# Kernel optimization log

Measured on AMD Instinct MI355X. Metric: run time of the kernel, lower is better.

## Reference

```python
import jax, jax.numpy as jnp
import numpy as np

N, B, SDIM, ADIM, HID, HEADS = 8, 32768, 128, 16, 128, 4
AD = HID // HEADS  # attend_dim = 32
IDIM = SDIM + ADIM


def setup_inputs() -> dict:
    key = jax.random.key(0)
    ks = jax.random.split(key, 16)
    nrm = jax.random.normal
    return {
        "states": nrm(ks[0], (N, B, SDIM), jnp.float32),
        "actions": nrm(ks[1], (N, B, ADIM), jnp.float32),
        # per-agent critic encoder (Linear(idim, hid) + ReLU)
        "We": nrm(ks[2], (N, IDIM, HID), jnp.float32) * 0.05,
        "be": nrm(ks[3], (N, HID), jnp.float32) * 0.05,
        # per-agent state encoder (Linear(sdim, hid) + ReLU)
        "Ws": nrm(ks[4], (N, SDIM, HID), jnp.float32) * 0.05,
        "bs": nrm(ks[5], (N, HID), jnp.float32) * 0.05,
        # per-head extractors (shared across agents)
        "Wk": nrm(ks[6], (HEADS, HID, AD), jnp.float32) * 0.05,  # bias=False
        "Wq": nrm(ks[7], (HEADS, HID, AD), jnp.float32) * 0.05,  # bias=False
        "Wv": nrm(ks[8], (HEADS, HID, AD), jnp.float32) * 0.05,
        "bv": nrm(ks[9], (HEADS, AD), jnp.float32) * 0.05,
        # per-agent critic head: Linear(2*hid, hid) + ReLU + Linear(hid, adim)
        "Wc1": nrm(ks[10], (N, 2 * HID, HID), jnp.float32) * 0.05,
        "bc1": nrm(ks[11], (N, HID), jnp.float32) * 0.05,
        "Wc2": nrm(ks[12], (N, HID, ADIM), jnp.float32) * 0.05,
        "bc2": nrm(ks[13], (N, ADIM), jnp.float32) * 0.05,
    }


def reference(states, actions, We, be, Ws, bs, Wk, Wq, Wv, bv, Wc1, bc1, Wc2, bc2):
    # encoders
    inp = jnp.concatenate([states, actions], axis=-1)                      # [N,B,idim]
    sa_enc = jax.nn.relu(jnp.einsum('nbi,nih->nbh', inp, We) + be[:, None, :])
    s_enc = jax.nn.relu(jnp.einsum('nbs,nsh->nbh', states, Ws) + bs[:, None, :])
    # per-head keys/values/selectors; k = head index
    K = jnp.einsum('nbh,khd->knbd', sa_enc, Wk)                            # [H,N,B,ad]
    V = jax.nn.relu(jnp.einsum('nbh,khd->knbd', sa_enc, Wv) + bv[:, None, None, :])
    Q = jnp.einsum('nbh,khd->knbd', s_enc, Wq)
    # attention logits: selector of agent i dotted with key of agent j
    logits = jnp.einsum('kibd,kjbd->kbij', Q, K) / np.sqrt(AD).astype(np.float32)
    # exclude-self masking (equivalent to stacking keys with j != i)
    self_mask = jnp.eye(N, dtype=bool)                                     # [N,N]
    masked = jnp.where(self_mask[None, None, :, :], jnp.float32(-1e9), logits)
    attn = jax.nn.softmax(masked, axis=-1)                                 # [H,B,N,N]
    other = jnp.einsum('kbij,kjbd->ikbd', attn, V)                         # [N,H,B,ad]
    other = other.transpose(0, 2, 1, 3).reshape(N, B, HEADS * AD)          # head-order concat
    # per-agent critic MLP
    critic_in = jnp.concatenate([s_enc, other], axis=-1)                   # [N,B,2*hid]
    h1 = jax.nn.relu(jnp.einsum('nbc,nch->nbh', critic_in, Wc1) + bc1[:, None, :])
    all_q = jnp.einsum('nbh,nha->nba', h1, Wc2) + bc2[:, None, :]          # [N,B,adim]
    int_acs = jnp.argmax(actions, axis=-1)                                 # [N,B]
    q = jnp.take_along_axis(all_q, int_acs[..., None], axis=-1)            # [N,B,1]
    return q
```

## Files before the change

### kernel.cpp

```cpp
#include <hip/hip_runtime.h>

#define NAG 8
#define BB 32768
#define SDIM 128
#define ADIM 16
#define HID 128
#define IDIM 144

typedef unsigned short u16;
typedef unsigned int u32;
typedef __attribute__((ext_vector_type(8))) short short8;
typedef __attribute__((ext_vector_type(4))) float floatx4;

__device__ __forceinline__ u16 f2bf(float f) {
  u32 u = __float_as_uint(f);
  u32 r = (u + 0x7FFFu + ((u >> 16) & 1u)) >> 16;
  return (u16)r;
}
__device__ __forceinline__ float bflo(u32 u) { return __uint_as_float(u << 16); }
__device__ __forceinline__ float bfhi(u32 u) { return __uint_as_float(u & 0xFFFF0000u); }


__global__ void prep_kernel(const float* __restrict__ We, const float* __restrict__ Ws,
                            const float* __restrict__ Wk, const float* __restrict__ Wq,
                            const float* __restrict__ Wv, const float* __restrict__ Wc1,
                            u16* __restrict__ ws) {
  int idx = blockIdx.x * 256 + threadIdx.x;
  const float* src;
  u16* dst;
  int e, Kreal, mode = 0;
  if (idx < 163840) {
    int a = idx / 20480; e = idx % 20480;
    src = We + a * (IDIM * HID); dst = ws + a * 20480; Kreal = IDIM;
  } else if (idx < 294912) {
    int r = idx - 163840; int a = r >> 14; e = r & 16383;
    src = Ws + a * 16384; dst = ws + 163840 + a * 16384; Kreal = 128;
  } else if (idx < 311296) {
    e = idx - 294912; src = Wk; dst = ws + 294912; Kreal = 128; mode = 1;
  } else if (idx < 327680) {
    e = idx - 311296; src = Wv; dst = ws + 311296; Kreal = 128; mode = 1;
  } else if (idx < 344064) {
    e = idx - 327680; src = Wq; dst = ws + 327680; Kreal = 128; mode = 1;
  } else if (idx < 606208) {
    int r = idx - 344064; int a = r >> 15; e = r & 32767;
    src = Wc1 + a * 32768; dst = ws + 344064 + a * 32768; Kreal = 256;
  } else {
    return;
  }
  int j = e & 7, lane = (e >> 3) & 63, ct = (e >> 9) & 7, kc = e >> 12;
  int k = kc * 32 + ((lane >> 4) << 3) + j;
  int c = ct * 16 + (lane & 15);
  float val = 0.f;
  if (k < Kreal)
    val = mode ? src[((c >> 5) * 128 + k) * 32 + (c & 31)]
               : src[k * 128 + c];
  dst[e] = f2bf(val);
}

template <int NKC>
__device__ __forceinline__ void gemm8(const u16* A, const int astride,
                                      const u16* __restrict__ W,
                                      const int wave, const int lane, floatx4* acc) {
  const int arow = wave * 16 + (lane & 15);
  const int koff = (lane >> 4) << 3;
#pragma unroll
  for (int kc = 0; kc < NKC; ++kc) {
    short8 a = *(const short8*)&A[arow * astride + kc * 32 + koff];
#pragma unroll
    for (int ct = 0; ct < 8; ++ct) {
      short8 b = *(const short8*)&W[kc * 4096 + ct * 512 + lane * 8];
      acc[ct] = __builtin_amdgcn_mfma_f32_16x16x32_bf16(a, b, acc[ct], 0, 0, 0);
    }
  }
}

__global__ __launch_bounds__(512, 4) void k1_kernel(
    const float* __restrict__ states, const float* __restrict__ actions,
    const float* __restrict__ be, const float* __restrict__ bs, const float* __restrict__ bv,
    const u16* __restrict__ wsbase,
    u16* __restrict__ Kbuf, u16* __restrict__ Vbuf, u16* __restrict__ Qbuf,
    u16* __restrict__ CI) {
  __shared__ __align__(16) u16 Alds[128 * 160];
  __shared__ __align__(16) u16 Ebuf[128 * 136];

  const int tid = threadIdx.x, lane = tid & 63, wave = tid >> 6;
  const int n = blockIdx.y;
  const size_t b0 = (size_t)blockIdx.x * 128;
  const int colb = lane & 15;
  const int rowl = wave * 16 + ((lane >> 4) << 2);

  const u16* WeP = wsbase + (size_t)n * 20480;
  const u16* WsP = wsbase + 163840 + (size_t)n * 16384;
  const u16* WkP = wsbase + 294912;
  const u16* WvP = wsbase + 311296;
  const u16* WqP = wsbase + 327680;

  {
    const float4* sp = (const float4*)(states + ((size_t)n * BB + b0) * SDIM);
#pragma unroll
    for (int it = 0; it < 8; ++it) {
      int c = tid + it * 512;
      float4 v = sp[c];
      int row = c >> 5, col = (c & 31) << 2;
      *(uint2*)&Alds[row * 160 + col] =
          make_uint2((u32)f2bf(v.x) | ((u32)f2bf(v.y) << 16),
                     (u32)f2bf(v.z) | ((u32)f2bf(v.w) << 16));
    }
    const float4* apt = (const float4*)(actions + ((size_t)n * BB + b0) * ADIM);
    {
      float4 v = apt[tid];
      int row = tid >> 2, col = 128 + ((tid & 3) << 2);
      *(uint2*)&Alds[row * 160 + col] =
          make_uint2((u32)f2bf(v.x) | ((u32)f2bf(v.y) << 16),
                     (u32)f2bf(v.z) | ((u32)f2bf(v.w) << 16));
    }
    {
      int row = tid >> 2, col = 144 + ((tid & 3) << 2);
      *(uint2*)&Alds[row * 160 + col] = make_uint2(0u, 0u);
    }
  }
  __syncthreads();

  floatx4 acc[8];

#pragma unroll
  for (int ct = 0; ct < 8; ++ct) acc[ct] = (floatx4){0.f, 0.f, 0.f, 0.f};
  gemm8<5>(Alds, 160, WeP, wave, lane, acc);
#pragma unroll
  for (int ct = 0; ct < 8; ++ct) {
    int col = ct * 16 + colb;
    float bb = be[n * HID + col];
#pragma unroll
    for (int r = 0; r < 4; ++r)
      Ebuf[(rowl + r) * 136 + col] = f2bf(fmaxf(acc[ct][r] + bb, 0.f));
  }
  __syncthreads();

#pragma unroll
  for (int ct = 0; ct < 8; ++ct) acc[ct] = (floatx4){0.f, 0.f, 0.f, 0.f};
  gemm8<4>(Ebuf, 136, WkP, wave, lane, acc);
#pragma unroll
  for (int ct = 0; ct < 8; ++ct) {
    int col = ct * 16 + colb;
#pragma unroll
    for (int r = 0; r < 4; ++r)
      Kbuf[((size_t)n * BB + b0 + rowl + r) * HID + col] = f2bf(acc[ct][r]);
  }

#pragma unroll
  for (int ct = 0; ct < 8; ++ct) acc[ct] = (floatx4){0.f, 0.f, 0.f, 0.f};
  gemm8<4>(Ebuf, 136, WvP, wave, lane, acc);
#pragma unroll
  for (int ct = 0; ct < 8; ++ct) {
    int col = ct * 16 + colb;
    float bb = bv[col];
#pragma unroll
    for (int r = 0; r < 4; ++r)
      Vbuf[((size_t)n * BB + b0 + rowl + r) * HID + col] = f2bf(fmaxf(acc[ct][r] + bb, 0.f));
  }

#pragma unroll
  for (int ct = 0; ct < 8; ++ct) acc[ct] = (floatx4){0.f, 0.f, 0.f, 0.f};
  gemm8<4>(Alds, 160, WsP, wave, lane, acc);
  u16 e2u[32];
#pragma unroll
  for (int ct = 0; ct < 8; ++ct) {
    int col = ct * 16 + colb;
    float bb = bs[n * HID + col];
#pragma unroll
    for (int r = 0; r < 4; ++r) {
      u16 u = f2bf(fmaxf(acc[ct][r] + bb, 0.f));
      e2u[ct * 4 + r] = u;
      CI[((size_t)n * BB + b0 + rowl + r) * 256 + col] = u;
    }
  }
  __syncthreads();

#pragma unroll
  for (int ct = 0; ct < 8; ++ct) {
    int col = ct * 16 + colb;
#pragma unroll
    for (int r = 0; r < 4; ++r)
      Ebuf[(rowl + r) * 136 + col] = e2u[ct * 4 + r];
  }
  __syncthreads();

#pragma unroll
  for (int ct = 0; ct < 8; ++ct) acc[ct] = (floatx4){0.f, 0.f, 0.f, 0.f};
  gemm8<4>(Ebuf, 136, WqP, wave, lane, acc);
#pragma unroll
  for (int ct = 0; ct < 8; ++ct) {
    int col = ct * 16 + colb;
#pragma unroll
    for (int r = 0; r < 4; ++r)
      Qbuf[((size_t)n * BB + b0 + rowl + r) * HID + col] = f2bf(acc[ct][r]);
  }
}

__global__ __launch_bounds__(512, 4) void k2_kernel(const u16* __restrict__ Kb,
                                                    const u16* __restrict__ Vb,
                                                    const u16* __restrict__ Qb,
                                                    u16* __restrict__ CI) {
  __shared__ __align__(16) u16 Ksh[8 * 16 * 128];
  __shared__ __align__(16) u16 Vsh[8 * 16 * 128];

  const int tid = threadIdx.x;
  const int i = tid >> 6;
  const int lane = tid & 63;
  const int h = lane >> 4;
  const int b = lane & 15;
  const size_t b0 = (size_t)blockIdx.x * 16;
  const float scale = 0.17677669529663687f;

  {
    uint4* kd = (uint4*)Ksh;
    uint4* vd = (uint4*)Vsh;
#pragma unroll
    for (int it = 0; it < 4; ++it) {
      int l = tid + it * 512;
      int j = l >> 8, bs_ = (l >> 4) & 15, t = l & 15;
      size_t gidx = ((size_t)j * BB + b0 + bs_) * 16 + t;
      int slot = (t + bs_) & 15;
      int didx = (j * 16 + bs_) * 16 + slot;
      kd[didx] = ((const uint4*)Kb)[gidx];
      vd[didx] = ((const uint4*)Vb)[gidx];
    }
  }
  __syncthreads();

  float q[32];
  {
    const u32* qp = (const u32*)(Qb + ((size_t)i * BB + b0 + b) * HID + h * 32);
#pragma unroll
    for (int t = 0; t < 16; ++t) {
      u32 u = qp[t];
      q[2 * t] = bflo(u);
      q[2 * t + 1] = bfhi(u);
    }
  }

  float lg[8];
#pragma unroll
  for (int j = 0; j < 8; ++j) {
    if (j != i) {
      float acc = 0.f;
#pragma unroll
      for (int c = 0; c < 4; ++c) {
        int slot = ((h * 4 + c) + b) & 15;
        uint4 kv = *(const uint4*)&Ksh[((j * 16 + b) * 16 + slot) * 8];
        const u32 kw[4] = {kv.x, kv.y, kv.z, kv.w};
#pragma unroll
        for (int t = 0; t < 4; ++t) {
          int d = c * 8 + t * 2;
          acc = fmaf(bflo(kw[t]), q[d], acc);
          acc = fmaf(bfhi(kw[t]), q[d + 1], acc);
        }
      }
      lg[j] = acc * scale;
    } else {
      lg[j] = -1e9f;
    }
  }

  float m = lg[0];
#pragma unroll
  for (int j = 1; j < 8; ++j) m = fmaxf(m, lg[j]);
  float p[8], s = 0.f;
#pragma unroll
  for (int j = 0; j < 8; ++j) {
    p[j] = __expf(lg[j] - m);
    s += p[j];
  }
  const float inv = 1.f / s;

  float o[32];
#pragma unroll
  for (int d = 0; d < 32; ++d) o[d] = 0.f;
#pragma unroll
  for (int j = 0; j < 8; ++j) {
    if (j == i) continue;
    const float pj = p[j] * inv;
#pragma unroll
    for (int c = 0; c < 4; ++c) {
      int slot = ((h * 4 + c) + b) & 15;
      uint4 vv = *(const uint4*)&Vsh[((j * 16 + b) * 16 + slot) * 8];
      const u32 vw[4] = {vv.x, vv.y, vv.z, vv.w};
#pragma unroll
      for (int t = 0; t < 4; ++t) {
        int d = c * 8 + t * 2;
        o[d] = fmaf(pj, bflo(vw[t]), o[d]);
        o[d + 1] = fmaf(pj, bfhi(vw[t]), o[d + 1]);
      }
    }
  }

  u32 ow[16];
#pragma unroll
  for (int t = 0; t < 16; ++t)
    ow[t] = (u32)f2bf(o[2 * t]) | ((u32)f2bf(o[2 * t + 1]) << 16);
  uint4* op = (uint4*)(CI + ((size_t)i * BB + b0 + b) * 256 + 128 + h * 32);
  op[0] = make_uint4(ow[0], ow[1], ow[2], ow[3]);
  op[1] = make_uint4(ow[4], ow[5], ow[6], ow[7]);
  op[2] = make_uint4(ow[8], ow[9], ow[10], ow[11]);
  op[3] = make_uint4(ow[12], ow[13], ow[14], ow[15]);
}

__global__ __launch_bounds__(512, 4) void k3_kernel(
    const u16* __restrict__ CI, const u16* __restrict__ Wc1P, const float* __restrict__ bc1,
    const float* __restrict__ Wc2, const float* __restrict__ bc2,
    const float* __restrict__ actions, float* __restrict__ out) {
  __shared__ __align__(16) u16 Alds[128 * 264];
  __shared__ __align__(16) float Wc2s[2048];

  const int tid = threadIdx.x, lane = tid & 63, wave = tid >> 6;
  const int n = blockIdx.y;
  const size_t b0 = (size_t)blockIdx.x * 128;
  const int colb = lane & 15;
  const int rowl = wave * 16 + ((lane >> 4) << 2);

  {
    const uint4* src = (const uint4*)(CI + ((size_t)n * BB + b0) * 256);
    uint4* dstA = (uint4*)Alds;
#pragma unroll
    for (int it = 0; it < 8; ++it) {
      int c = tid + it * 512;
      int row = c >> 5, c16 = c & 31;
      dstA[row * 33 + c16] = src[c];
    }
    ((float4*)Wc2s)[tid] = ((const float4*)(Wc2 + n * 2048))[tid];
  }
  __syncthreads();

  floatx4 acc[8];
#pragma unroll
  for (int ct = 0; ct < 8; ++ct) acc[ct] = (floatx4){0.f, 0.f, 0.f, 0.f};
  gemm8<8>(Alds, 264, Wc1P + (size_t)n * 32768, wave, lane, acc);
  __syncthreads();

#pragma unroll
  for (int ct = 0; ct < 8; ++ct) {
    int col = ct * 16 + colb;
    float bb = bc1[n * HID + col];
#pragma unroll
    for (int r = 0; r < 4; ++r) {
      float v = fmaxf(acc[ct][r] + bb, 0.f);
      Alds[(rowl + r) * 136 + col] = f2bf(v);
    }
  }
  __syncthreads();

  {
    const int bloc = tid >> 2, part = tid & 3;
    const size_t b = b0 + bloc;
    const float* ap = actions + ((size_t)n * BB + b) * ADIM;
    int am = 0;
    float mv = ap[0];
#pragma unroll
    for (int t = 1; t < 16; ++t) {
      float v = ap[t];
      if (v > mv) { mv = v; am = t; }
    }
    float a2 = 0.f;
    const int cb = part * 32;
#pragma unroll
    for (int c2 = 0; c2 < 32; ++c2) {
      float hv = __uint_as_float((u32)Alds[bloc * 136 + cb + c2] << 16);
      a2 = fmaf(hv, Wc2s[(cb + c2) * 16 + am], a2);
    }
    a2 += __shfl_xor(a2, 1);
    a2 += __shfl_xor(a2, 2);
    if (part == 0) out[(size_t)n * BB + b] = a2 + bc2[n * ADIM + am];
  }
}

extern "C" void kernel_launch(void* const* d_in, const int* in_sizes, int n_in,
                              void* d_out, int out_size, void* d_ws, size_t ws_size,
                              hipStream_t stream) {
  const float* states  = (const float*)d_in[0];
  const float* actions = (const float*)d_in[1];
  const float* We  = (const float*)d_in[2];
  const float* be  = (const float*)d_in[3];
  const float* Ws  = (const float*)d_in[4];
  const float* bs  = (const float*)d_in[5];
  const float* Wk  = (const float*)d_in[6];
  const float* Wq  = (const float*)d_in[7];
  const float* Wv  = (const float*)d_in[8];
  const float* bv  = (const float*)d_in[9];
  const float* Wc1 = (const float*)d_in[10];
  const float* bc1 = (const float*)d_in[11];
  const float* Wc2 = (const float*)d_in[12];
  const float* bc2 = (const float*)d_in[13];
  float* out = (float*)d_out;
  u16* ws = (u16*)d_ws;

  u16* Kbuf = ws + 606208;
  u16* Vbuf = ws + 34160640;
  u16* Qbuf = ws + 67715072;
  u16* CI   = ws + 101269504;

  prep_kernel<<<2368, 256, 0, stream>>>(We, Ws, Wk, Wq, Wv, Wc1, ws);
  k1_kernel<<<dim3(256, 8), 512, 0, stream>>>(states, actions, be, bs, bv, ws,
                                              Kbuf, Vbuf, Qbuf, CI);
  k2_kernel<<<2048, 512, 0, stream>>>(Kbuf, Vbuf, Qbuf, CI);
  k3_kernel<<<dim3(256, 8), 512, 0, stream>>>(CI, ws + 344064, bc1, Wc2, bc2, actions, out);
}
```

Before: 493.3 us.

## Swap GEMM wave tiling to column-per-wave with register-resident weight fragments

Each wave now owns one 16-column output slice across all 128 rows, so its weight fragments for every K chunk are loaded once into registers and reused across eight row tiles, instead of re-reading weights for each row tile. In k1 the states and actions tiles are no longer staged through LDS as bf16; the A fragments are read straight from global fp32 and converted in registers, which removes the Alds buffer and one barrier. The cost is that states are read from global twice (once for the We GEMM, once for the Ws GEMM) with strided per-lane loads, and register pressure rises from holding the weight fragments.

New measurement: 645.5 us. 30.8% more time.

```diff
diff --git a/kernel.cpp b/kernel.cpp
--- a/kernel.cpp
+++ b/kernel.cpp
@@ -12,6 +12,8 @@
 typedef __attribute__((ext_vector_type(8))) short short8;
 typedef __attribute__((ext_vector_type(4))) float floatx4;
 
+#define BMFMA(a, b, c) __builtin_amdgcn_mfma_f32_16x16x32_bf16((a), (b), (c), 0, 0, 0)
+
 __device__ __forceinline__ u16 f2bf(float f) {
   u32 u = __float_as_uint(f);
   u32 r = (u + 0x7FFFu + ((u >> 16) & 1u)) >> 16;
@@ -19,6 +21,15 @@
 }
 __device__ __forceinline__ float bflo(u32 u) { return __uint_as_float(u << 16); }
 __device__ __forceinline__ float bfhi(u32 u) { return __uint_as_float(u & 0xFFFF0000u); }
+
+__device__ __forceinline__ short8 cvt8(const float4 a, const float4 b) {
+  short8 r;
+  r[0] = (short)f2bf(a.x); r[1] = (short)f2bf(a.y);
+  r[2] = (short)f2bf(a.z); r[3] = (short)f2bf(a.w);
+  r[4] = (short)f2bf(b.x); r[5] = (short)f2bf(b.y);
+  r[6] = (short)f2bf(b.z); r[7] = (short)f2bf(b.w);
+  return r;
+}
 
 
 __global__ void prep_kernel(const float* __restrict__ We, const float* __restrict__ Ws,
@@ -57,143 +68,161 @@
   dst[e] = f2bf(val);
 }
 
-template <int NKC>
-__device__ __forceinline__ void gemm8(const u16* A, const int astride,
-                                      const u16* __restrict__ W,
-                                      const int wave, const int lane, floatx4* acc) {
-  const int arow = wave * 16 + (lane & 15);
-  const int koff = (lane >> 4) << 3;
-#pragma unroll
-  for (int kc = 0; kc < NKC; ++kc) {
-    short8 a = *(const short8*)&A[arow * astride + kc * 32 + koff];
-#pragma unroll
-    for (int ct = 0; ct < 8; ++ct) {
-      short8 b = *(const short8*)&W[kc * 4096 + ct * 512 + lane * 8];
-      acc[ct] = __builtin_amdgcn_mfma_f32_16x16x32_bf16(a, b, acc[ct], 0, 0, 0);
-    }
-  }
-}
-
 __global__ __launch_bounds__(512, 4) void k1_kernel(
     const float* __restrict__ states, const float* __restrict__ actions,
     const float* __restrict__ be, const float* __restrict__ bs, const float* __restrict__ bv,
     const u16* __restrict__ wsbase,
     u16* __restrict__ Kbuf, u16* __restrict__ Vbuf, u16* __restrict__ Qbuf,
     u16* __restrict__ CI) {
-  __shared__ __align__(16) u16 Alds[128 * 160];
   __shared__ __align__(16) u16 Ebuf[128 * 136];
 
-  const int tid = threadIdx.x, lane = tid & 63, wave = tid >> 6;
+  const int tid = threadIdx.x, lane = tid & 63, w = tid >> 6;
   const int n = blockIdx.y;
   const size_t b0 = (size_t)blockIdx.x * 128;
-  const int colb = lane & 15;
-  const int rowl = wave * 16 + ((lane >> 4) << 2);
-
-  const u16* WeP = wsbase + (size_t)n * 20480;
-  const u16* WsP = wsbase + 163840 + (size_t)n * 16384;
-  const u16* WkP = wsbase + 294912;
-  const u16* WvP = wsbase + 311296;
-  const u16* WqP = wsbase + 327680;
-
-  {
-    const float4* sp = (const float4*)(states + ((size_t)n * BB + b0) * SDIM);
-#pragma unroll
-    for (int it = 0; it < 8; ++it) {
-      int c = tid + it * 512;
-      float4 v = sp[c];
-      int row = c >> 5, col = (c & 31) << 2;
-      *(uint2*)&Alds[row * 160 + col] =
-          make_uint2((u32)f2bf(v.x) | ((u32)f2bf(v.y) << 16),
-                     (u32)f2bf(v.z) | ((u32)f2bf(v.w) << 16));
-    }
-    const float4* apt = (const float4*)(actions + ((size_t)n * BB + b0) * ADIM);
-    {
-      float4 v = apt[tid];
-      int row = tid >> 2, col = 128 + ((tid & 3) << 2);
-      *(uint2*)&Alds[row * 160 + col] =
-          make_uint2((u32)f2bf(v.x) | ((u32)f2bf(v.y) << 16),
-                     (u32)f2bf(v.z) | ((u32)f2bf(v.w) << 16));
-    }
-    {
-      int row = tid >> 2, col = 144 + ((tid & 3) << 2);
-      *(uint2*)&Alds[row * 160 + col] = make_uint2(0u, 0u);
-    }
-  }
-  __syncthreads();
+  const int cb = lane & 15, qq = lane >> 4;
+  const int col = w * 16 + cb;
+  const int ar = lane & 15;
+  const int koff = qq * 8;
+
+  const u16* WeF = wsbase + (size_t)n * 20480 + w * 512 + (size_t)lane * 8;
+  const u16* WsF = wsbase + 163840 + (size_t)n * 16384 + w * 512 + (size_t)lane * 8;
+  const u16* WkF = wsbase + 294912 + w * 512 + (size_t)lane * 8;
+  const u16* WvF = wsbase + 311296 + w * 512 + (size_t)lane * 8;
+  const u16* WqF = wsbase + 327680 + w * 512 + (size_t)lane * 8;
+
+  const float* Sb = states + ((size_t)n * BB + b0) * SDIM;
+  const float* Ab = actions + ((size_t)n * BB + b0) * ADIM;
+  const size_t orow = (size_t)n * BB + b0;
 
   floatx4 acc[8];
 
-#pragma unroll
-  for (int ct = 0; ct < 8; ++ct) acc[ct] = (floatx4){0.f, 0.f, 0.f, 0.f};
-  gemm8<5>(Alds, 160, WeP, wave, lane, acc);
-#pragma unroll
-  for (int ct = 0; ct < 8; ++ct) {
-    int col = ct * 16 + colb;
-    float bb = be[n * HID + col];
+  {
+    short8 wf[5];
+#pragma unroll
+    for (int kc = 0; kc < 5; ++kc) wf[kc] = *(const short8*)(WeF + kc * 4096);
+#pragma unroll
+    for (int m = 0; m < 8; ++m) acc[m] = (floatx4){0.f, 0.f, 0.f, 0.f};
+#pragma unroll
+    for (int m = 0; m < 8; ++m) {
+      const float* sp = Sb + (size_t)(16 * m + ar) * SDIM + koff;
+#pragma unroll
+      for (int kc = 0; kc < 4; ++kc) {
+        float4 x = *(const float4*)(sp + kc * 32);
+        float4 y = *(const float4*)(sp + kc * 32 + 4);
+        acc[m] = BMFMA(cvt8(x, y), wf[kc], acc[m]);
+      }
+      short8 af = {0, 0, 0, 0, 0, 0, 0, 0};
+      if (qq < 2) {
+        const float* ap = Ab + (size_t)(16 * m + ar) * ADIM + koff;
+        float4 x = *(const float4*)ap;
+        float4 y = *(const float4*)(ap + 4);
+        af = cvt8(x, y);
+      }
+      acc[m] = BMFMA(af, wf[4], acc[m]);
+    }
+    const float bb = be[n * HID + col];
+#pragma unroll
+    for (int m = 0; m < 8; ++m)
+#pragma unroll
+      for (int r = 0; r < 4; ++r)
+        Ebuf[(16 * m + qq * 4 + r) * 136 + col] = f2bf(fmaxf(acc[m][r] + bb, 0.f));
+  }
+  __syncthreads();
+
+  {
+    short8 wf[4];
+#pragma unroll
+    for (int kc = 0; kc < 4; ++kc) wf[kc] = *(const short8*)(WkF + kc * 4096);
+#pragma unroll
+    for (int m = 0; m < 8; ++m) acc[m] = (floatx4){0.f, 0.f, 0.f, 0.f};
+#pragma unroll
+    for (int m = 0; m < 8; ++m)
+#pragma unroll
+      for (int kc = 0; kc < 4; ++kc) {
+        short8 a = *(const short8*)&Ebuf[(16 * m + ar) * 136 + kc * 32 + koff];
+        acc[m] = BMFMA(a, wf[kc], acc[m]);
+      }
+#pragma unroll
+    for (int m = 0; m < 8; ++m)
+#pragma unroll
+      for (int r = 0; r < 4; ++r)
+        Kbuf[(orow + 16 * m + qq * 4 + r) * HID + col] = f2bf(acc[m][r]);
+  }
+
+  {
+    short8 wf[4];
+#pragma unroll
+    for (int kc = 0; kc < 4; ++kc) wf[kc] = *(const short8*)(WvF + kc * 4096);
+#pragma unroll
+    for (int m = 0; m < 8; ++m) acc[m] = (floatx4){0.f, 0.f, 0.f, 0.f};
+#pragma unroll
+    for (int m = 0; m < 8; ++m)
+#pragma unroll
+      for (int kc = 0; kc < 4; ++kc) {
+        short8 a = *(const short8*)&Ebuf[(16 * m + ar) * 136 + kc * 32 + koff];
+        acc[m] = BMFMA(a, wf[kc], acc[m]);
+      }
+    const float bb = bv[col];
+#pragma unroll
+    for (int m = 0; m < 8; ++m)
+#pragma unroll
+      for (int r = 0; r < 4; ++r)
+        Vbuf[(orow + 16 * m + qq * 4 + r) * HID + col] = f2bf(fmaxf(acc[m][r] + bb, 0.f));
+  }
+
+  {
+    short8 wf[4];
+#pragma unroll
+    for (int kc = 0; kc < 4; ++kc) wf[kc] = *(const short8*)(WsF + kc * 4096);
+#pragma unroll
+    for (int m = 0; m < 8; ++m) acc[m] = (floatx4){0.f, 0.f, 0.f, 0.f};
+#pragma unroll
+    for (int m = 0; m < 8; ++m) {
+      const float* sp = Sb + (size_t)(16 * m + ar) * SDIM + koff;
+#pragma unroll
+      for (int kc = 0; kc < 4; ++kc) {
+        float4 x = *(const float4*)(sp + kc * 32);
+        float4 y = *(const float4*)(sp + kc * 32 + 4);
+        acc[m] = BMFMA(cvt8(x, y), wf[kc], acc[m]);
+      }
+    }
+    const float bb = bs[n * HID + col];
+#pragma unroll
+    for (int m = 0; m < 8; ++m)
+#pragma unroll
+      for (int r = 0; r < 4; ++r) {
+        float v = fmaxf(acc[m][r] + bb, 0.f);
+        acc[m][r] = v;
+        CI[(orow + 16 * m + qq * 4 + r) * 256 + col] = f2bf(v);
+      }
+  }
+  __syncthreads();
+
+#pragma unroll
+  for (int m = 0; m < 8; ++m)
 #pragma unroll
     for (int r = 0; r < 4; ++r)
-      Ebuf[(rowl + r) * 136 + col] = f2bf(fmaxf(acc[ct][r] + bb, 0.f));
-  }
-  __syncthreads();
-
-#pragma unroll
-  for (int ct = 0; ct < 8; ++ct) acc[ct] = (floatx4){0.f, 0.f, 0.f, 0.f};
-  gemm8<4>(Ebuf, 136, WkP, wave, lane, acc);
-#pragma unroll
-  for (int ct = 0; ct < 8; ++ct) {
-    int col = ct * 16 + colb;
-#pragma unroll
-    for (int r = 0; r < 4; ++r)
-      Kbuf[((size_t)n * BB + b0 + rowl + r) * HID + col] = f2bf(acc[ct][r]);
-  }
-
-#pragma unroll
-  for (int ct = 0; ct < 8; ++ct) acc[ct] = (floatx4){0.f, 0.f, 0.f, 0.f};
-  gemm8<4>(Ebuf, 136, WvP, wave, lane, acc);
-#pragma unroll
-  for (int ct = 0; ct < 8; ++ct) {
-    int col = ct * 16 + colb;
-    float bb = bv[col];
-#pragma unroll
-    for (int r = 0; r < 4; ++r)
-      Vbuf[((size_t)n * BB + b0 + rowl + r) * HID + col] = f2bf(fmaxf(acc[ct][r] + bb, 0.f));
-  }
-
-#pragma unroll
-  for (int ct = 0; ct < 8; ++ct) acc[ct] = (floatx4){0.f, 0.f, 0.f, 0.f};
-  gemm8<4>(Alds, 160, WsP, wave, lane, acc);
-  u16 e2u[32];
-#pragma unroll
-  for (int ct = 0; ct < 8; ++ct) {
-    int col = ct * 16 + colb;
-    float bb = bs[n * HID + col];
-#pragma unroll
-    for (int r = 0; r < 4; ++r) {
-      u16 u = f2bf(fmaxf(acc[ct][r] + bb, 0.f));
-      e2u[ct * 4 + r] = u;
-      CI[((size_t)n * BB + b0 + rowl + r) * 256 + col] = u;
-    }
-  }
-  __syncthreads();
-
-#pragma unroll
-  for (int ct = 0; ct < 8; ++ct) {
-    int col = ct * 16 + colb;
-#pragma unroll
-    for (int r = 0; r < 4; ++r)
-      Ebuf[(rowl + r) * 136 + col] = e2u[ct * 4 + r];
-  }
-  __syncthreads();
-
-#pragma unroll
-  for (int ct = 0; ct < 8; ++ct) acc[ct] = (floatx4){0.f, 0.f, 0.f, 0.f};
-  gemm8<4>(Ebuf, 136, WqP, wave, lane, acc);
-#pragma unroll
-  for (int ct = 0; ct < 8; ++ct) {
-    int col = ct * 16 + colb;
-#pragma unroll
-    for (int r = 0; r < 4; ++r)
-      Qbuf[((size_t)n * BB + b0 + rowl + r) * HID + col] = f2bf(acc[ct][r]);
+      Ebuf[(16 * m + qq * 4 + r) * 136 + col] = f2bf(acc[m][r]);
+  __syncthreads();
+
+  {
+    short8 wf[4];
+#pragma unroll
+    for (int kc = 0; kc < 4; ++kc) wf[kc] = *(const short8*)(WqF + kc * 4096);
+#pragma unroll
+    for (int m = 0; m < 8; ++m) acc[m] = (floatx4){0.f, 0.f, 0.f, 0.f};
+#pragma unroll
+    for (int m = 0; m < 8; ++m)
+#pragma unroll
+      for (int kc = 0; kc < 4; ++kc) {
+        short8 a = *(const short8*)&Ebuf[(16 * m + ar) * 136 + kc * 32 + koff];
+        acc[m] = BMFMA(a, wf[kc], acc[m]);
+      }
+#pragma unroll
+    for (int m = 0; m < 8; ++m)
+#pragma unroll
+      for (int r = 0; r < 4; ++r)
+        Qbuf[(orow + 16 * m + qq * 4 + r) * HID + col] = f2bf(acc[m][r]);
   }
 }
 
@@ -312,11 +341,13 @@
   __shared__ __align__(16) u16 Alds[128 * 264];
   __shared__ __align__(16) float Wc2s[2048];
 
-  const int tid = threadIdx.x, lane = tid & 63, wave = tid >> 6;
+  const int tid = threadIdx.x, lane = tid & 63, w = tid >> 6;
   const int n = blockIdx.y;
   const size_t b0 = (size_t)blockIdx.x * 128;
-  const int colb = lane & 15;
-  const int rowl = wave * 16 + ((lane >> 4) << 2);
+  const int cb = lane & 15, qq = lane >> 4;
+  const int col = w * 16 + cb;
+  const int ar = lane & 15;
+  const int koff = qq * 8;
 
   {
     const uint4* src = (const uint4*)(CI + ((size_t)n * BB + b0) * 256);
@@ -332,20 +363,30 @@
   __syncthreads();
 
   floatx4 acc[8];
-#pragma unroll
-  for (int ct = 0; ct < 8; ++ct) acc[ct] = (floatx4){0.f, 0.f, 0.f, 0.f};
-  gemm8<8>(Alds, 264, Wc1P + (size_t)n * 32768, wave, lane, acc);
-  __syncthreads();
-
-#pragma unroll
-  for (int ct = 0; ct < 8; ++ct) {
-    int col = ct * 16 + colb;
-    float bb = bc1[n * HID + col];
-#pragma unroll
-    for (int r = 0; r < 4; ++r) {
-      float v = fmaxf(acc[ct][r] + bb, 0.f);
-      Alds[(rowl + r) * 136 + col] = f2bf(v);
-    }
+  {
+    const u16* WcF = Wc1P + (size_t)n * 32768 + w * 512 + (size_t)lane * 8;
+    short8 wf[8];
+#pragma unroll
+    for (int kc = 0; kc < 8; ++kc) wf[kc] = *(const short8*)(WcF + kc * 4096);
+#pragma unroll
+    for (int m = 0; m < 8; ++m) acc[m] = (floatx4){0.f, 0.f, 0.f, 0.f};
+#pragma unroll
+    for (int m = 0; m < 8; ++m)
+#pragma unroll
+      for (int kc = 0; kc < 8; ++kc) {
+        short8 a = *(const short8*)&Alds[(16 * m + ar) * 264 + kc * 32 + koff];
+        acc[m] = BMFMA(a, wf[kc], acc[m]);
+      }
+  }
+  __syncthreads();
+
+  {
+    const float bb = bc1[n * HID + col];
+#pragma unroll
+    for (int m = 0; m < 8; ++m)
+#pragma unroll
+      for (int r = 0; r < 4; ++r)
+        Alds[(16 * m + qq * 4 + r) * 136 + col] = f2bf(fmaxf(acc[m][r] + bb, 0.f));
   }
   __syncthreads();
 
@@ -361,11 +402,11 @@
       if (v > mv) { mv = v; am = t; }
     }
     float a2 = 0.f;
-    const int cb = part * 32;
+    const int cbk = part * 32;
 #pragma unroll
     for (int c2 = 0; c2 < 32; ++c2) {
-      float hv = __uint_as_float((u32)Alds[bloc * 136 + cb + c2] << 16);
-      a2 = fmaf(hv, Wc2s[(cb + c2) * 16 + am], a2);
+      float hv = __uint_as_float((u32)Alds[bloc * 136 + cbk + c2] << 16);
+      a2 = fmaf(hv, Wc2s[(cbk + c2) * 16 + am], a2);
     }
     a2 += __shfl_xor(a2, 1);
     a2 += __shfl_xor(a2, 2);
```

## Stage weights in LDS and keep activations in registers as MFMA B operand

Applied to the files above, without the earlier changes.

k1 and k3 now stage each weight matrix into shared memory per phase and load activation fragments directly from global into registers, swapping MFMA operand roles so activations are the B operand. The GEMM output lands transposed, so each lane holds one row's contiguous four columns and can do packed 8-byte stores. k3 also folds the second linear layer and the argmax gather into registers with cross-lane shuffles, dropping the LDS round trip. Weights were previously read from global on every MFMA; this trades that for more barriers and repeated weight staging per block.

Result: faster. 420.3 us (-14.8%).

```diff
diff --git a/kernel.cpp b/kernel.cpp
--- a/kernel.cpp
+++ b/kernel.cpp
@@ -12,6 +12,8 @@
 typedef __attribute__((ext_vector_type(8))) short short8;
 typedef __attribute__((ext_vector_type(4))) float floatx4;
 
+#define BMFMA(a, b, c) __builtin_amdgcn_mfma_f32_16x16x32_bf16((a), (b), (c), 0, 0, 0)
+
 __device__ __forceinline__ u16 f2bf(float f) {
   u32 u = __float_as_uint(f);
   u32 r = (u + 0x7FFFu + ((u >> 16) & 1u)) >> 16;
@@ -19,6 +21,26 @@
 }
 __device__ __forceinline__ float bflo(u32 u) { return __uint_as_float(u << 16); }
 __device__ __forceinline__ float bfhi(u32 u) { return __uint_as_float(u & 0xFFFF0000u); }
+
+__device__ __forceinline__ short8 cvt8(const float4 a, const float4 b) {
+  short8 r;
+  r[0] = (short)f2bf(a.x); r[1] = (short)f2bf(a.y);
+  r[2] = (short)f2bf(a.z); r[3] = (short)f2bf(a.w);
+  r[4] = (short)f2bf(b.x); r[5] = (short)f2bf(b.y);
+  r[6] = (short)f2bf(b.z); r[7] = (short)f2bf(b.w);
+  return r;
+}
+__device__ __forceinline__ uint2 pack4(float a, float b, float c, float d) {
+  return make_uint2((u32)f2bf(a) | ((u32)f2bf(b) << 16),
+                    (u32)f2bf(c) | ((u32)f2bf(d) << 16));
+}
+
+__device__ __forceinline__ void stageW(u16* Wb, const u16* __restrict__ src, int nu4, int tid) {
+  const uint4* s4 = (const uint4*)src;
+  uint4* d4 = (uint4*)Wb;
+#pragma unroll 1
+  for (int it = tid; it < nu4; it += 512) d4[it] = s4[it];
+}
 
 
 __global__ void prep_kernel(const float* __restrict__ We, const float* __restrict__ Ws,
@@ -57,37 +79,21 @@
   dst[e] = f2bf(val);
 }
 
-template <int NKC>
-__device__ __forceinline__ void gemm8(const u16* A, const int astride,
-                                      const u16* __restrict__ W,
-                                      const int wave, const int lane, floatx4* acc) {
-  const int arow = wave * 16 + (lane & 15);
-  const int koff = (lane >> 4) << 3;
-#pragma unroll
-  for (int kc = 0; kc < NKC; ++kc) {
-    short8 a = *(const short8*)&A[arow * astride + kc * 32 + koff];
-#pragma unroll
-    for (int ct = 0; ct < 8; ++ct) {
-      short8 b = *(const short8*)&W[kc * 4096 + ct * 512 + lane * 8];
-      acc[ct] = __builtin_amdgcn_mfma_f32_16x16x32_bf16(a, b, acc[ct], 0, 0, 0);
-    }
-  }
-}
-
 __global__ __launch_bounds__(512, 4) void k1_kernel(
     const float* __restrict__ states, const float* __restrict__ actions,
     const float* __restrict__ be, const float* __restrict__ bs, const float* __restrict__ bv,
     const u16* __restrict__ wsbase,
     u16* __restrict__ Kbuf, u16* __restrict__ Vbuf, u16* __restrict__ Qbuf,
     u16* __restrict__ CI) {
-  __shared__ __align__(16) u16 Alds[128 * 160];
-  __shared__ __align__(16) u16 Ebuf[128 * 136];
-
-  const int tid = threadIdx.x, lane = tid & 63, wave = tid >> 6;
+  __shared__ __align__(16) u16 Wb[20480];
+  __shared__ __align__(16) u16 Est[8 * 16 * 136];
+
+  const int tid = threadIdx.x, lane = tid & 63, w = tid >> 6;
+  const int cb = lane & 15, qq = lane >> 4;
   const int n = blockIdx.y;
   const size_t b0 = (size_t)blockIdx.x * 128;
-  const int colb = lane & 15;
-  const int rowl = wave * 16 + ((lane >> 4) << 2);
+  const size_t grow = (size_t)n * BB + b0 + w * 16 + cb;
+  u16* stw = Est + w * (16 * 136) + cb * 136;
 
   const u16* WeP = wsbase + (size_t)n * 20480;
   const u16* WsP = wsbase + 163840 + (size_t)n * 16384;
@@ -95,105 +101,103 @@
   const u16* WvP = wsbase + 311296;
   const u16* WqP = wsbase + 327680;
 
+  stageW(Wb, WeP, 2560, tid);
+  short8 xf[5];
   {
-    const float4* sp = (const float4*)(states + ((size_t)n * BB + b0) * SDIM);
-#pragma unroll
-    for (int it = 0; it < 8; ++it) {
-      int c = tid + it * 512;
-      float4 v = sp[c];
-      int row = c >> 5, col = (c & 31) << 2;
-      *(uint2*)&Alds[row * 160 + col] =
-          make_uint2((u32)f2bf(v.x) | ((u32)f2bf(v.y) << 16),
-                     (u32)f2bf(v.z) | ((u32)f2bf(v.w) << 16));
-    }
-    const float4* apt = (const float4*)(actions + ((size_t)n * BB + b0) * ADIM);
-    {
-      float4 v = apt[tid];
-      int row = tid >> 2, col = 128 + ((tid & 3) << 2);
-      *(uint2*)&Alds[row * 160 + col] =
-          make_uint2((u32)f2bf(v.x) | ((u32)f2bf(v.y) << 16),
-                     (u32)f2bf(v.z) | ((u32)f2bf(v.w) << 16));
-    }
-    {
-      int row = tid >> 2, col = 144 + ((tid & 3) << 2);
-      *(uint2*)&Alds[row * 160 + col] = make_uint2(0u, 0u);
-    }
-  }
-  __syncthreads();
-
-  floatx4 acc[8];
-
-#pragma unroll
-  for (int ct = 0; ct < 8; ++ct) acc[ct] = (floatx4){0.f, 0.f, 0.f, 0.f};
-  gemm8<5>(Alds, 160, WeP, wave, lane, acc);
-#pragma unroll
-  for (int ct = 0; ct < 8; ++ct) {
-    int col = ct * 16 + colb;
-    float bb = be[n * HID + col];
-#pragma unroll
-    for (int r = 0; r < 4; ++r)
-      Ebuf[(rowl + r) * 136 + col] = f2bf(fmaxf(acc[ct][r] + bb, 0.f));
-  }
-  __syncthreads();
-
-#pragma unroll
-  for (int ct = 0; ct < 8; ++ct) acc[ct] = (floatx4){0.f, 0.f, 0.f, 0.f};
-  gemm8<4>(Ebuf, 136, WkP, wave, lane, acc);
-#pragma unroll
-  for (int ct = 0; ct < 8; ++ct) {
-    int col = ct * 16 + colb;
-#pragma unroll
-    for (int r = 0; r < 4; ++r)
-      Kbuf[((size_t)n * BB + b0 + rowl + r) * HID + col] = f2bf(acc[ct][r]);
-  }
-
-#pragma unroll
-  for (int ct = 0; ct < 8; ++ct) acc[ct] = (floatx4){0.f, 0.f, 0.f, 0.f};
-  gemm8<4>(Ebuf, 136, WvP, wave, lane, acc);
-#pragma unroll
-  for (int ct = 0; ct < 8; ++ct) {
-    int col = ct * 16 + colb;
-    float bb = bv[col];
-#pragma unroll
-    for (int r = 0; r < 4; ++r)
-      Vbuf[((size_t)n * BB + b0 + rowl + r) * HID + col] = f2bf(fmaxf(acc[ct][r] + bb, 0.f));
-  }
-
-#pragma unroll
-  for (int ct = 0; ct < 8; ++ct) acc[ct] = (floatx4){0.f, 0.f, 0.f, 0.f};
-  gemm8<4>(Alds, 160, WsP, wave, lane, acc);
-  u16 e2u[32];
-#pragma unroll
-  for (int ct = 0; ct < 8; ++ct) {
-    int col = ct * 16 + colb;
-    float bb = bs[n * HID + col];
-#pragma unroll
-    for (int r = 0; r < 4; ++r) {
-      u16 u = f2bf(fmaxf(acc[ct][r] + bb, 0.f));
-      e2u[ct * 4 + r] = u;
-      CI[((size_t)n * BB + b0 + rowl + r) * 256 + col] = u;
-    }
-  }
-  __syncthreads();
-
-#pragma unroll
-  for (int ct = 0; ct < 8; ++ct) {
-    int col = ct * 16 + colb;
-#pragma unroll
-    for (int r = 0; r < 4; ++r)
-      Ebuf[(rowl + r) * 136 + col] = e2u[ct * 4 + r];
-  }
-  __syncthreads();
-
-#pragma unroll
-  for (int ct = 0; ct < 8; ++ct) acc[ct] = (floatx4){0.f, 0.f, 0.f, 0.f};
-  gemm8<4>(Ebuf, 136, WqP, wave, lane, acc);
-#pragma unroll
-  for (int ct = 0; ct < 8; ++ct) {
-    int col = ct * 16 + colb;
-#pragma unroll
-    for (int r = 0; r < 4; ++r)
-      Qbuf[((size_t)n * BB + b0 + rowl + r) * HID + col] = f2bf(acc[ct][r]);
+    const float* sp = states + grow * SDIM + qq * 8;
+#pragma unroll
+    for (int kc = 0; kc < 4; ++kc) {
+      float4 x = *(const float4*)(sp + kc * 32);
+      float4 y = *(const float4*)(sp + kc * 32 + 4);
+      xf[kc] = cvt8(x, y);
+    }
+    xf[4] = (short8){0, 0, 0, 0, 0, 0, 0, 0};
+    if (qq < 2) {
+      const float* ap = actions + grow * ADIM + qq * 8;
+      xf[4] = cvt8(*(const float4*)ap, *(const float4*)(ap + 4));
+    }
+  }
+  __syncthreads();
+#pragma unroll
+  for (int ct = 0; ct < 8; ++ct) {
+    floatx4 a = (floatx4){0.f, 0.f, 0.f, 0.f};
+#pragma unroll
+    for (int kc = 0; kc < 5; ++kc) {
+      short8 wfr = *(const short8*)&Wb[(kc * 8 + ct) * 512 + lane * 8];
+      a = BMFMA(wfr, xf[kc], a);
+    }
+    floatx4 bb = *(const floatx4*)&be[n * HID + ct * 16 + qq * 4];
+    *(uint2*)&stw[ct * 16 + qq * 4] =
+        pack4(fmaxf(a[0] + bb[0], 0.f), fmaxf(a[1] + bb[1], 0.f),
+              fmaxf(a[2] + bb[2], 0.f), fmaxf(a[3] + bb[3], 0.f));
+  }
+  __syncthreads();
+
+  stageW(Wb, WkP, 2048, tid);
+  short8 ef[4];
+#pragma unroll
+  for (int kc = 0; kc < 4; ++kc) ef[kc] = *(const short8*)&stw[kc * 32 + qq * 8];
+  __syncthreads();
+#pragma unroll
+  for (int ct = 0; ct < 8; ++ct) {
+    floatx4 a = (floatx4){0.f, 0.f, 0.f, 0.f};
+#pragma unroll
+    for (int kc = 0; kc < 4; ++kc) {
+      short8 wfr = *(const short8*)&Wb[(kc * 8 + ct) * 512 + lane * 8];
+      a = BMFMA(wfr, ef[kc], a);
+    }
+    *(uint2*)&Kbuf[grow * HID + ct * 16 + qq * 4] = pack4(a[0], a[1], a[2], a[3]);
+  }
+  __syncthreads();
+
+  stageW(Wb, WvP, 2048, tid);
+  __syncthreads();
+#pragma unroll
+  for (int ct = 0; ct < 8; ++ct) {
+    floatx4 a = (floatx4){0.f, 0.f, 0.f, 0.f};
+#pragma unroll
+    for (int kc = 0; kc < 4; ++kc) {
+      short8 wfr = *(const short8*)&Wb[(kc * 8 + ct) * 512 + lane * 8];
+      a = BMFMA(wfr, ef[kc], a);
+    }
+    floatx4 bb = *(const floatx4*)&bv[ct * 16 + qq * 4];
+    *(uint2*)&Vbuf[grow * HID + ct * 16 + qq * 4] =
+        pack4(fmaxf(a[0] + bb[0], 0.f), fmaxf(a[1] + bb[1], 0.f),
+              fmaxf(a[2] + bb[2], 0.f), fmaxf(a[3] + bb[3], 0.f));
+  }
+  __syncthreads();
+
+  stageW(Wb, WsP, 2048, tid);
+  __syncthreads();
+#pragma unroll
+  for (int ct = 0; ct < 8; ++ct) {
+    floatx4 a = (floatx4){0.f, 0.f, 0.f, 0.f};
+#pragma unroll
+    for (int kc = 0; kc < 4; ++kc) {
+      short8 wfr = *(const short8*)&Wb[(kc * 8 + ct) * 512 + lane * 8];
+      a = BMFMA(wfr, xf[kc], a);
+    }
+    floatx4 bb = *(const floatx4*)&bs[n * HID + ct * 16 + qq * 4];
+    uint2 pk = pack4(fmaxf(a[0] + bb[0], 0.f), fmaxf(a[1] + bb[1], 0.f),
+                     fmaxf(a[2] + bb[2], 0.f), fmaxf(a[3] + bb[3], 0.f));
+    *(uint2*)&CI[grow * 256 + ct * 16 + qq * 4] = pk;
+    *(uint2*)&stw[ct * 16 + qq * 4] = pk;
+  }
+  __syncthreads();
+
+  stageW(Wb, WqP, 2048, tid);
+#pragma unroll
+  for (int kc = 0; kc < 4; ++kc) ef[kc] = *(const short8*)&stw[kc * 32 + qq * 8];
+  __syncthreads();
+#pragma unroll
+  for (int ct = 0; ct < 8; ++ct) {
+    floatx4 a = (floatx4){0.f, 0.f, 0.f, 0.f};
+#pragma unroll
+    for (int kc = 0; kc < 4; ++kc) {
+      short8 wfr = *(const short8*)&Wb[(kc * 8 + ct) * 512 + lane * 8];
+      a = BMFMA(wfr, ef[kc], a);
+    }
+    *(uint2*)&Qbuf[grow * HID + ct * 16 + qq * 4] = pack4(a[0], a[1], a[2], a[3]);
   }
 }
 
@@ -309,68 +313,74 @@
     const u16* __restrict__ CI, const u16* __restrict__ Wc1P, const float* __restrict__ bc1,
     const float* __restrict__ Wc2, const float* __restrict__ bc2,
     const float* __restrict__ actions, float* __restrict__ out) {
-  __shared__ __align__(16) u16 Alds[128 * 264];
+  __shared__ __align__(16) u16 Wb[16384];
   __shared__ __align__(16) float Wc2s[2048];
 
-  const int tid = threadIdx.x, lane = tid & 63, wave = tid >> 6;
+  const int tid = threadIdx.x, lane = tid & 63, w = tid >> 6;
+  const int cb = lane & 15, qq = lane >> 4;
   const int n = blockIdx.y;
   const size_t b0 = (size_t)blockIdx.x * 128;
-  const int colb = lane & 15;
-  const int rowl = wave * 16 + ((lane >> 4) << 2);
-
-  {
-    const uint4* src = (const uint4*)(CI + ((size_t)n * BB + b0) * 256);
-    uint4* dstA = (uint4*)Alds;
-#pragma unroll
-    for (int it = 0; it < 8; ++it) {
-      int c = tid + it * 512;
-      int row = c >> 5, c16 = c & 31;
-      dstA[row * 33 + c16] = src[c];
-    }
-    ((float4*)Wc2s)[tid] = ((const float4*)(Wc2 + n * 2048))[tid];
-  }
-  __syncthreads();
+  const size_t grow = (size_t)n * BB + b0 + w * 16 + cb;
+
+  const u16* W1 = Wc1P + (size_t)n * 32768;
+  Wc2s[tid] = Wc2[n * 2048 + tid];
+  Wc2s[tid + 512] = Wc2[n * 2048 + tid + 512];
+  Wc2s[tid + 1024] = Wc2[n * 2048 + tid + 1024];
+  Wc2s[tid + 1536] = Wc2[n * 2048 + tid + 1536];
+  stageW(Wb, W1, 2048, tid);
+
+  const u16* cip = CI + grow * 256;
+  short8 cf[4];
+#pragma unroll
+  for (int kc = 0; kc < 4; ++kc) cf[kc] = *(const short8*)(cip + kc * 32 + qq * 8);
 
   floatx4 acc[8];
 #pragma unroll
   for (int ct = 0; ct < 8; ++ct) acc[ct] = (floatx4){0.f, 0.f, 0.f, 0.f};
-  gemm8<8>(Alds, 264, Wc1P + (size_t)n * 32768, wave, lane, acc);
-  __syncthreads();
-
-#pragma unroll
-  for (int ct = 0; ct < 8; ++ct) {
-    int col = ct * 16 + colb;
-    float bb = bc1[n * HID + col];
+
+  __syncthreads();
+#pragma unroll
+  for (int ct = 0; ct < 8; ++ct)
+#pragma unroll
+    for (int kc = 0; kc < 4; ++kc) {
+      short8 wfr = *(const short8*)&Wb[(kc * 8 + ct) * 512 + lane * 8];
+      acc[ct] = BMFMA(wfr, cf[kc], acc[ct]);
+    }
+  __syncthreads();
+  stageW(Wb, W1 + 16384, 2048, tid);
+#pragma unroll
+  for (int kc = 0; kc < 4; ++kc) cf[kc] = *(const short8*)(cip + 128 + kc * 32 + qq * 8);
+  __syncthreads();
+#pragma unroll
+  for (int ct = 0; ct < 8; ++ct)
+#pragma unroll
+    for (int kc = 0; kc < 4; ++kc) {
+      short8 wfr = *(const short8*)&Wb[(kc * 8 + ct) * 512 + lane * 8];
+      acc[ct] = BMFMA(wfr, cf[kc], acc[ct]);
+    }
+
+  const float* ap = actions + grow * ADIM;
+  int am = 0;
+  float mv = ap[0];
+#pragma unroll
+  for (int t = 1; t < 16; ++t) {
+    float v = ap[t];
+    if (v > mv) { mv = v; am = t; }
+  }
+
+  float a2 = 0.f;
+#pragma unroll
+  for (int ct = 0; ct < 8; ++ct) {
+    floatx4 bb = *(const floatx4*)&bc1[n * HID + ct * 16 + qq * 4];
 #pragma unroll
     for (int r = 0; r < 4; ++r) {
-      float v = fmaxf(acc[ct][r] + bb, 0.f);
-      Alds[(rowl + r) * 136 + col] = f2bf(v);
-    }
-  }
-  __syncthreads();
-
-  {
-    const int bloc = tid >> 2, part = tid & 3;
-    const size_t b = b0 + bloc;
-    const float* ap = actions + ((size_t)n * BB + b) * ADIM;
-    int am = 0;
-    float mv = ap[0];
-#pragma unroll
-    for (int t = 1; t < 16; ++t) {
-      float v = ap[t];
-      if (v > mv) { mv = v; am = t; }
-    }
-    float a2 = 0.f;
-    const int cb = part * 32;
-#pragma unroll
-    for (int c2 = 0; c2 < 32; ++c2) {
-      float hv = __uint_as_float((u32)Alds[bloc * 136 + cb + c2] << 16);
-      a2 = fmaf(hv, Wc2s[(cb + c2) * 16 + am], a2);
-    }
-    a2 += __shfl_xor(a2, 1);
-    a2 += __shfl_xor(a2, 2);
-    if (part == 0) out[(size_t)n * BB + b] = a2 + bc2[n * ADIM + am];
-  }
+      float h = fmaxf(acc[ct][r] + bb[r], 0.f);
+      a2 = fmaf(h, Wc2s[(ct * 16 + qq * 4 + r) * 16 + am], a2);
+    }
+  }
+  a2 += __shfl_xor(a2, 16);
+  a2 += __shfl_xor(a2, 32);
+  if (qq == 0) out[grow] = a2 + bc2[n * ADIM + am];
 }
 
 extern "C" void kernel_launch(void* const* d_in, const int* in_sizes, int n_in,
```
